# Kernel tuning notes

Hardware: AMD Instinct MI355X
Metric: run time of the kernel (lower is better)

Reference implementation:

```python
import jax, jax.numpy as jnp
import numpy as np

HEADS = 4
ATTN_MODE = 'strided'
LOCAL_ATTN_CTX = 32
BLOCKSIZE = 32


def strided_transpose(x, n_ctx, local_attn_ctx):
    # [n, t, e] -> [n, bT_ctx, local, e] -> [n, local, bT_ctx, e] -> [n, t, e]
    bT_ctx = n_ctx // local_attn_ctx
    n, t, e = x.shape
    x = x.reshape(n, bT_ctx, local_attn_ctx, e)
    x = jnp.transpose(x, (0, 2, 1, 3))
    return x.reshape(n, t, e)


def setup_inputs() -> dict:
    key = jax.random.key(0)
    kq, kk, kv = jax.random.split(key, 3)
    shape = (2, 4096, 1024)
    return {
        'q': jax.random.normal(kq, shape, dtype=jnp.float32),
        'k': jax.random.normal(kk, shape, dtype=jnp.float32),
        'v': jax.random.normal(kv, shape, dtype=jnp.float32),
    }


def reference(q, k, v):
    n_ctx = q.shape[1]
    if ATTN_MODE == 'strided':
        bT_ctx = n_ctx // LOCAL_ATTN_CTX
        assert bT_ctx % BLOCKSIZE == 0
        q = strided_transpose(q, n_ctx, LOCAL_ATTN_CTX)
        k = strided_transpose(k, n_ctx, LOCAL_ATTN_CTX)
        v = strided_transpose(v, n_ctx, LOCAL_ATTN_CTX)
    n_state = q.shape[-1] // HEADS
    scale = 1.0 / np.sqrt(n_state)
    w = jnp.einsum('nte,nse->nts', q, k)            # [n, t, t] full scores
    w = jax.nn.softmax(w * scale, axis=-1)
    a = jnp.einsum('nts,nse->nte', w, v)
    if ATTN_MODE == 'strided':
        n, t, e = a.shape
        bT_ctx = n_ctx // LOCAL_ATTN_CTX
        a = a.reshape(n, LOCAL_ATTN_CTX, bT_ctx, e)
        a = jnp.transpose(a, (0, 2, 1, 3))
        a = a.reshape(n, t, e)
    return a
```

## Files before the change

kernel.cpp:

```cpp
#include <hip/hip_runtime.h>

using short8  = __attribute__((ext_vector_type(8))) short;
using ushort8 = __attribute__((ext_vector_type(8))) unsigned short;
using f32x4   = __attribute__((ext_vector_type(4))) float;

#define T 4096
#define E 1024
#define NB 2
#define BM 128
#define BN 128
#define BK 32

__device__ __forceinline__ unsigned short f2bf(float f) {
    unsigned int u = __builtin_bit_cast(unsigned int, f);
    u = (u + 0x7FFFu + ((u >> 16) & 1u)) >> 16;
    return (unsigned short)u;
}
__device__ __forceinline__ float bf2f(unsigned short h) {
    unsigned int u = ((unsigned int)h) << 16;
    return __builtin_bit_cast(float, u);
}

__device__ __forceinline__ void gld16(const unsigned short* g, unsigned short* l) {
    __builtin_amdgcn_global_load_lds(
        (__attribute__((address_space(1))) void*)g,
        (__attribute__((address_space(3))) void*)l, 16, 0, 0);
}

__global__ __launch_bounds__(256) void prologue(const float* __restrict__ q,
                                                const float* __restrict__ k,
                                                unsigned short* __restrict__ qb,
                                                unsigned short* __restrict__ kb,
                                                float* __restrict__ lsum) {
    int bid = blockIdx.x;
    if (bid < 8192) {
        const float* src = (bid < 4096) ? q : k;
        unsigned short* dst = (bid < 4096) ? qb : kb;
        size_t i = ((size_t)(bid & 4095) * 256 + threadIdx.x) * 8;
        float4 f0 = *(const float4*)(src + i);
        float4 f1 = *(const float4*)(src + i + 4);
        ushort8 u;
        u[0]=f2bf(f0.x); u[1]=f2bf(f0.y); u[2]=f2bf(f0.z); u[3]=f2bf(f0.w);
        u[4]=f2bf(f1.x); u[5]=f2bf(f1.y); u[6]=f2bf(f1.z); u[7]=f2bf(f1.w);
        *(ushort8*)(dst + i) = u;
    } else {
        lsum[(bid - 8192) * 256 + threadIdx.x] = 0.0f;
    }
}

__global__ __launch_bounds__(256) void v_transpose(const float* __restrict__ v,
                                                   unsigned short* __restrict__ vt) {
    __shared__ float tile[64][65];
    int id  = blockIdx.x;
    int b   = id / (64 * 16);
    int rem = id % (64 * 16);
    int t0  = (rem / 16) * 64;
    int e0  = (rem % 16) * 64;
    int tid = threadIdx.x;
    int r   = tid >> 2;
    int c0  = (tid & 3) * 16;
    const float* src = v + ((size_t)(b * T + t0 + r)) * E + e0 + c0;
    #pragma unroll
    for (int i = 0; i < 4; i++) {
        float4 f = *(const float4*)(src + i * 4);
        tile[r][c0 + i*4 + 0] = f.x;
        tile[r][c0 + i*4 + 1] = f.y;
        tile[r][c0 + i*4 + 2] = f.z;
        tile[r][c0 + i*4 + 3] = f.w;
    }
    __syncthreads();
    int er = tid >> 2;
    #pragma unroll
    for (int ch = 0; ch < 2; ch++) {
        int tl = (tid & 3) * 16 + ch * 8;
        ushort8 u;
        #pragma unroll
        for (int j = 0; j < 8; j++) u[j] = f2bf(tile[tl + j][er]);
        *(ushort8*)(vt + ((size_t)(b * E + e0 + er)) * T + t0 + tl) = u;
    }
}

template <int KITERS>
__device__ __forceinline__ void gemm_core(const unsigned short* Abase, int apitch,
                                          const unsigned short* Bbase, int bpitch,
                                          unsigned short* ldsA, unsigned short* ldsB,
                                          int tid, f32x4 (&acc)[4][4]) {
    const int lane = tid & 63, wave = tid >> 6;
    const int l15 = lane & 15, kq = lane >> 4;
    const int wm = (wave & 1) * 64, wn = (wave >> 1) * 64;

    const unsigned short* ga[2];
    const unsigned short* gb[2];
    unsigned short* la[2];
    unsigned short* lb[2];
    #pragma unroll
    for (int i = 0; i < 2; i++) {
        int p  = i * 256 + tid;
        int r  = p >> 2;
        int kqw = (p & 3) ^ ((p >> 3) & 3);
        ga[i] = Abase + (size_t)r * apitch + kqw * 8;
        gb[i] = Bbase + (size_t)r * bpitch + kqw * 8;
        la[i] = ldsA + (i * 256 + wave * 64) * 8;
        lb[i] = ldsB + (i * 256 + wave * 64) * 8;
    }
    int aoff[4], boff[4];
    #pragma unroll
    for (int mi = 0; mi < 4; mi++) {
        int r = wm + mi * 16 + l15;
        aoff[mi] = (r * 4 + (kq ^ ((r >> 1) & 3))) * 8;
        int rn = wn + mi * 16 + l15;
        boff[mi] = (rn * 4 + (kq ^ ((rn >> 1) & 3))) * 8;
    }

    for (int kt = 0; kt < KITERS; kt++) {
        __syncthreads();
        gld16(ga[0] + kt * BK, la[0]);
        gld16(ga[1] + kt * BK, la[1]);
        gld16(gb[0] + kt * BK, lb[0]);
        gld16(gb[1] + kt * BK, lb[1]);
        __syncthreads();
        short8 af[4], bf[4];
        #pragma unroll
        for (int i = 0; i < 4; i++) {
            af[i] = *(const short8*)(ldsA + aoff[i]);
            bf[i] = *(const short8*)(ldsB + boff[i]);
        }
        #pragma unroll
        for (int mi = 0; mi < 4; mi++)
            #pragma unroll
            for (int ni = 0; ni < 4; ni++)
                acc[mi][ni] = __builtin_amdgcn_mfma_f32_16x16x32_bf16(af[mi], bf[ni], acc[mi][ni], 0, 0, 0);
    }
}

__global__ __launch_bounds__(256, 2) void pass1(const unsigned short* __restrict__ qb,
                                                const unsigned short* __restrict__ kb,
                                                unsigned short* __restrict__ P,
                                                float* __restrict__ lsum) {
    __shared__ unsigned short ldsA[BM * BK];
    __shared__ unsigned short ldsB[BN * BK];
    const int bx = blockIdx.x;
    const int b = bx >> 10, mt = (bx >> 5) & 31, nt = bx & 31;
    const int tid = threadIdx.x;

    f32x4 acc[4][4];
    #pragma unroll
    for (int i = 0; i < 4; i++)
        #pragma unroll
        for (int j = 0; j < 4; j++) acc[i][j] = {};

    gemm_core<E / BK>(qb + ((size_t)b * T + mt * BM) * E, E,
                      kb + ((size_t)b * T + nt * BN) * E, E,
                      ldsA, ldsB, tid, acc);

    const int lane = tid & 63, wave = tid >> 6;
    const int wm = (wave & 1) * 64, wn = (wave >> 1) * 64;
    const int quad = lane >> 4, l15 = lane & 15;
    const float sl2 = 0.0625f * 1.44269504089f;
    const int col0 = nt * BN + wn + l15;

    #pragma unroll
    for (int mi = 0; mi < 4; mi++) {
        #pragma unroll
        for (int r = 0; r < 4; r++) {
            int row = mt * BM + wm + mi * 16 + quad * 4 + r;
            size_t base = ((size_t)b * T + row) * T + col0;
            float s = 0.0f;
            #pragma unroll
            for (int ni = 0; ni < 4; ni++) {
                float p = exp2f(acc[mi][ni][r] * sl2 - 12.0f);
                unsigned short h = f2bf(p);
                P[base + ni * 16] = h;
                s += bf2f(h);
            }
            s += __shfl_xor(s, 1);
            s += __shfl_xor(s, 2);
            s += __shfl_xor(s, 4);
            s += __shfl_xor(s, 8);
            if (l15 == 0) atomicAdd(lsum + b * T + row, s);
        }
    }
}

__global__ __launch_bounds__(256, 2) void pass2(const unsigned short* __restrict__ P,
                                                const unsigned short* __restrict__ vt,
                                                const float* __restrict__ lsum,
                                                float* __restrict__ out) {
    __shared__ unsigned short ldsA[BM * BK];
    __shared__ unsigned short ldsB[BN * BK];
    const int bx = blockIdx.x;
    const int b = bx >> 8, mt = (bx >> 3) & 31, nt = bx & 7;
    const int tid = threadIdx.x;

    f32x4 acc[4][4];
    #pragma unroll
    for (int i = 0; i < 4; i++)
        #pragma unroll
        for (int j = 0; j < 4; j++) acc[i][j] = {};

    gemm_core<T / BK>(P + ((size_t)b * T + mt * BM) * T, T,
                      vt + ((size_t)b * E + nt * BN) * T, T,
                      ldsA, ldsB, tid, acc);

    const int lane = tid & 63, wave = tid >> 6;
    const int wm = (wave & 1) * 64, wn = (wave >> 1) * 64;
    const int quad = lane >> 4, l15 = lane & 15;
    const int col0 = nt * BN + wn + l15;

    #pragma unroll
    for (int mi = 0; mi < 4; mi++) {
        #pragma unroll
        for (int r = 0; r < 4; r++) {
            int row = mt * BM + wm + mi * 16 + quad * 4 + r;
            float rl = 1.0f / lsum[b * T + row];
            size_t base = ((size_t)b * T + row) * E + col0;
            #pragma unroll
            for (int ni = 0; ni < 4; ni++)
                out[base + ni * 16] = acc[mi][ni][r] * rl;
        }
    }
}

extern "C" void kernel_launch(void* const* d_in, const int* in_sizes, int n_in,
                              void* d_out, int out_size, void* d_ws, size_t ws_size,
                              hipStream_t stream) {
    const float* q = (const float*)d_in[0];
    const float* k = (const float*)d_in[1];
    const float* v = (const float*)d_in[2];
    float* out = (float*)d_out;

    float* lsum = (float*)d_ws;
    unsigned short* qbw = (unsigned short*)((char*)d_ws + 32768);
    unsigned short* kbw = qbw + (size_t)NB * T * E;
    unsigned short* Pw  = kbw + (size_t)NB * T * E;
    unsigned short* vtw = qbw;

    prologue<<<8224, 256, 0, stream>>>(q, k, qbw, kbw, lsum);
    pass1<<<NB * 32 * 32, 256, 0, stream>>>(qbw, kbw, Pw, lsum);
    v_transpose<<<NB * 64 * 16, 256, 0, stream>>>(v, vtw);
    pass2<<<NB * 32 * 8, 256, 0, stream>>>(Pw, vtw, lsum, out);
}
```

Baseline: 336.1 us.

## Multi-buffer LDS tiles with async prefetch and remap blocks for L2 locality

```diff
diff --git a/kernel.cpp b/kernel.cpp
--- a/kernel.cpp
+++ b/kernel.cpp
@@ -10,6 +10,7 @@
 #define BM 128
 #define BN 128
 #define BK 32
+#define TILE_ELEMS (BM * BK)
 
 __device__ __forceinline__ unsigned short f2bf(float f) {
     unsigned int u = __builtin_bit_cast(unsigned int, f);
@@ -80,28 +81,27 @@
     }
 }
 
-template <int KITERS>
+template <int KITERS, int NBUF>
 __device__ __forceinline__ void gemm_core(const unsigned short* Abase, int apitch,
                                           const unsigned short* Bbase, int bpitch,
                                           unsigned short* ldsA, unsigned short* ldsB,
                                           int tid, f32x4 (&acc)[4][4]) {
+    constexpr int D = NBUF - 1;
     const int lane = tid & 63, wave = tid >> 6;
     const int l15 = lane & 15, kq = lane >> 4;
     const int wm = (wave & 1) * 64, wn = (wave >> 1) * 64;
 
     const unsigned short* ga[2];
     const unsigned short* gb[2];
-    unsigned short* la[2];
-    unsigned short* lb[2];
+    int lo[2];
     #pragma unroll
     for (int i = 0; i < 2; i++) {
-        int p  = i * 256 + tid;
-        int r  = p >> 2;
+        int p = i * 256 + tid;
+        int r = p >> 2;
         int kqw = (p & 3) ^ ((p >> 3) & 3);
         ga[i] = Abase + (size_t)r * apitch + kqw * 8;
         gb[i] = Bbase + (size_t)r * bpitch + kqw * 8;
-        la[i] = ldsA + (i * 256 + wave * 64) * 8;
-        lb[i] = ldsB + (i * 256 + wave * 64) * 8;
+        lo[i] = (i * 256 + wave * 64) * 8;
     }
     int aoff[4], boff[4];
     #pragma unroll
@@ -112,24 +112,42 @@
         boff[mi] = (rn * 4 + (kq ^ ((rn >> 1) & 3))) * 8;
     }
 
+    #pragma unroll
+    for (int i = 0; i < D; i++) {
+        gld16(ga[0] + i * BK, ldsA + i * TILE_ELEMS + lo[0]);
+        gld16(ga[1] + i * BK, ldsA + i * TILE_ELEMS + lo[1]);
+        gld16(gb[0] + i * BK, ldsB + i * TILE_ELEMS + lo[0]);
+        gld16(gb[1] + i * BK, ldsB + i * TILE_ELEMS + lo[1]);
+    }
+
+    int cbuf = 0, pbuf = D, pkt = D;
     for (int kt = 0; kt < KITERS; kt++) {
-        __syncthreads();
-        gld16(ga[0] + kt * BK, la[0]);
-        gld16(ga[1] + kt * BK, la[1]);
-        gld16(gb[0] + kt * BK, lb[0]);
-        gld16(gb[1] + kt * BK, lb[1]);
-        __syncthreads();
+        asm volatile("s_barrier" ::: "memory");
+        gld16(ga[0] + pkt * BK, ldsA + pbuf * TILE_ELEMS + lo[0]);
+        gld16(ga[1] + pkt * BK, ldsA + pbuf * TILE_ELEMS + lo[1]);
+        gld16(gb[0] + pkt * BK, ldsB + pbuf * TILE_ELEMS + lo[0]);
+        gld16(gb[1] + pkt * BK, ldsB + pbuf * TILE_ELEMS + lo[1]);
+        if constexpr (D == 1) asm volatile("s_waitcnt vmcnt(4)" ::: "memory");
+        else                  asm volatile("s_waitcnt vmcnt(8)" ::: "memory");
+        asm volatile("s_barrier" ::: "memory");
+
+        const unsigned short* A = ldsA + cbuf * TILE_ELEMS;
+        const unsigned short* B = ldsB + cbuf * TILE_ELEMS;
         short8 af[4], bf[4];
         #pragma unroll
         for (int i = 0; i < 4; i++) {
-            af[i] = *(const short8*)(ldsA + aoff[i]);
-            bf[i] = *(const short8*)(ldsB + boff[i]);
+            af[i] = *(const short8*)(A + aoff[i]);
+            bf[i] = *(const short8*)(B + boff[i]);
         }
         #pragma unroll
         for (int mi = 0; mi < 4; mi++)
             #pragma unroll
             for (int ni = 0; ni < 4; ni++)
                 acc[mi][ni] = __builtin_amdgcn_mfma_f32_16x16x32_bf16(af[mi], bf[ni], acc[mi][ni], 0, 0, 0);
+
+        if (++cbuf == NBUF) cbuf = 0;
+        if (++pbuf == NBUF) pbuf = 0;
+        if (++pkt == KITERS) pkt = 0;
     }
 }
 
@@ -137,21 +155,24 @@
                                                 const unsigned short* __restrict__ kb,
                                                 unsigned short* __restrict__ P,
                                                 float* __restrict__ lsum) {
-    __shared__ unsigned short ldsA[BM * BK];
-    __shared__ unsigned short ldsB[BN * BK];
+    __shared__ unsigned short ldsA[2 * TILE_ELEMS];
+    __shared__ unsigned short ldsB[2 * TILE_ELEMS];
     const int bx = blockIdx.x;
-    const int b = bx >> 10, mt = (bx >> 5) & 31, nt = bx & 31;
+    const int x = bx & 7, j = bx >> 3;
+    const int gm = x * 8 + (j & 7);
+    const int nt = j >> 3;
+    const int b = gm >> 5, mt = gm & 31;
     const int tid = threadIdx.x;
 
     f32x4 acc[4][4];
     #pragma unroll
     for (int i = 0; i < 4; i++)
         #pragma unroll
-        for (int j = 0; j < 4; j++) acc[i][j] = {};
-
-    gemm_core<E / BK>(qb + ((size_t)b * T + mt * BM) * E, E,
-                      kb + ((size_t)b * T + nt * BN) * E, E,
-                      ldsA, ldsB, tid, acc);
+        for (int jj = 0; jj < 4; jj++) acc[i][jj] = {};
+
+    gemm_core<E / BK, 2>(qb + ((size_t)b * T + mt * BM) * E, E,
+                         kb + ((size_t)b * T + nt * BN) * E, E,
+                         ldsA, ldsB, tid, acc);
 
     const int lane = tid & 63, wave = tid >> 6;
     const int wm = (wave & 1) * 64, wn = (wave >> 1) * 64;
@@ -186,21 +207,24 @@
                                                 const unsigned short* __restrict__ vt,
                                                 const float* __restrict__ lsum,
                                                 float* __restrict__ out) {
-    __shared__ unsigned short ldsA[BM * BK];
-    __shared__ unsigned short ldsB[BN * BK];
+    __shared__ unsigned short ldsA[3 * TILE_ELEMS];
+    __shared__ unsigned short ldsB[3 * TILE_ELEMS];
     const int bx = blockIdx.x;
-    const int b = bx >> 8, mt = (bx >> 3) & 31, nt = bx & 7;
+    const int x = bx & 7, j = bx >> 3;
+    const int gm = x * 8 + (j & 7);
+    const int nt = j >> 3;
+    const int b = gm >> 5, mt = gm & 31;
     const int tid = threadIdx.x;
 
     f32x4 acc[4][4];
     #pragma unroll
     for (int i = 0; i < 4; i++)
         #pragma unroll
-        for (int j = 0; j < 4; j++) acc[i][j] = {};
-
-    gemm_core<T / BK>(P + ((size_t)b * T + mt * BM) * T, T,
-                      vt + ((size_t)b * E + nt * BN) * T, T,
-                      ldsA, ldsB, tid, acc);
+        for (int jj = 0; jj < 4; jj++) acc[i][jj] = {};
+
+    gemm_core<T / BK, 3>(P + ((size_t)b * T + mt * BM) * T, T,
+                         vt + ((size_t)b * E + nt * BN) * T, T,
+                         ldsA, ldsB, tid, acc);
 
     const int lane = tid & 63, wave = tid >> 6;
     const int wm = (wave & 1) * 64, wn = (wave >> 1) * 64;
```

Measured after the change: 313.0 us. -6.9%, faster.
